# Kernel tuning notes

Hardware: AMD Instinct MI355X
Metric: run time of the kernel (lower is better)

The kernel has to match this reference:

```python
import jax, jax.numpy as jnp
import numpy as np

QP = 127.0          # 2**(8-1)-1, signed symmetric int8
MIN_RANGE = 1e-6


def _ste_round(x):
    # round_pass: forward round, straight-through gradient
    return x + jax.lax.stop_gradient(jnp.round(x) - x)


def _quant_per_tensor(x):
    # symmetric per-tensor: scale = max|x| / Qp (grad flows through max as in source)
    scale = jnp.maximum(jnp.max(jnp.abs(x)), MIN_RANGE) / QP
    return _ste_round(x / scale), scale


def _qlinear(x2d, w, b):
    # faithful to _quantize_global (prefix_token_num=None path):
    #   out = (x_q @ w_q.T + bias) * (s_w * s_x)
    xq, sx = _quant_per_tensor(x2d)
    wq, sw = _quant_per_tensor(w)
    out = jnp.matmul(xq, wq.T) + b[None, :]
    return out * (sw * sx)


def setup_inputs() -> dict:
    key = jax.random.key(0)
    k = jax.random.split(key, 5)
    B, N, D, H = 8, 1024, 1024, 4096
    return {
        "x": jax.random.normal(k[0], (B, N, D), dtype=jnp.float32),
        "w1": jax.random.normal(k[1], (H, D), dtype=jnp.float32) * 0.02,
        "b1": jax.random.normal(k[2], (H,), dtype=jnp.float32) * 0.02,
        "w2": jax.random.normal(k[3], (D, H), dtype=jnp.float32) * 0.02,
        "b2": jax.random.normal(k[4], (D,), dtype=jnp.float32) * 0.02,
    }


def reference(x, w1, b1, w2, b2):
    B, N, D = x.shape
    h = _qlinear(x.reshape(-1, D), w1, b1)          # [B*N, H]
    h = jax.nn.gelu(h, approximate=False)            # exact GELU (nn.GELU default)
    o = _qlinear(h, w2, b2)                          # [B*N, D]
    return o.reshape(B, N, -1)
```

## Files before the change

### kernel.cpp

```cpp
#include <hip/hip_runtime.h>
#include <cstdint>
#include <cmath>

#define QP    127.0f
#define MINR  1e-6f

#define MTOK 8192
#define DDIM 1024
#define HDIM 4096

typedef __attribute__((ext_vector_type(4))) int int32x4;

__device__ __forceinline__ void gload16(const void* g, void* l) {
    __builtin_amdgcn_global_load_lds(
        (const __attribute__((address_space(1))) void*)g,
        (__attribute__((address_space(3))) void*)l, 16, 0, 0);
}

__global__ void zero_scales_kernel(float* g) {
    if (threadIdx.x < 4) g[threadIdx.x] = 0.0f;
}

__global__ void absmax_kernel(const float* __restrict__ in, int n4, float* __restrict__ gout) {
    const float4* in4 = (const float4*)in;
    int tid = blockIdx.x * blockDim.x + threadIdx.x;
    int stride = gridDim.x * blockDim.x;
    float m = 0.0f;
    for (int i = tid; i < n4; i += stride) {
        float4 v = in4[i];
        m = fmaxf(m, fmaxf(fmaxf(fabsf(v.x), fabsf(v.y)), fmaxf(fabsf(v.z), fabsf(v.w))));
    }
    #pragma unroll
    for (int off = 32; off; off >>= 1) m = fmaxf(m, __shfl_down(m, off));
    __shared__ float sm[4];
    int lane = threadIdx.x & 63, w = threadIdx.x >> 6;
    if (lane == 0) sm[w] = m;
    __syncthreads();
    if (threadIdx.x == 0) {
        float bm = fmaxf(fmaxf(sm[0], sm[1]), fmaxf(sm[2], sm[3]));
        atomicMax((int*)gout, __float_as_int(bm));
    }
}

__global__ void quant_kernel(const float* __restrict__ in, int8_t* __restrict__ out,
                             int n4, const float* __restrict__ gm) {
    const float s = fmaxf(*gm, MINR) / QP;
    const float4* in4 = (const float4*)in;
    int* out4 = (int*)out;
    int tid = blockIdx.x * blockDim.x + threadIdx.x;
    int stride = gridDim.x * blockDim.x;
    for (int i = tid; i < n4; i += stride) {
        float4 v = in4[i];
        int q0 = ((int)rintf(v.x / s)) & 255;
        int q1 = ((int)rintf(v.y / s)) & 255;
        int q2 = ((int)rintf(v.z / s)) & 255;
        int q3 = ((int)rintf(v.w / s)) & 255;
        out4[i] = q0 | (q1 << 8) | (q2 << 16) | (q3 << 24);
    }
}

template<int KD, int ND, bool GELU_EPI>
__global__ __launch_bounds__(256, 2)
void gemm_i8_kernel(const int8_t* __restrict__ A, const int8_t* __restrict__ B,
                    const float* __restrict__ bias,
                    const float* __restrict__ gmA, const float* __restrict__ gmB,
                    float* __restrict__ out, float* __restrict__ omax) {
    __shared__ int8_t lA[128 * 128];
    __shared__ int8_t lB[128 * 128];
    const int t = threadIdx.x;
    const int lane = t & 63;
    const int w = t >> 6;
    const int wm = (w >> 1) * 64;
    const int wn = (w & 1) * 64;
    const int lr = lane & 15;
    const int lg = lane >> 4;
    const int br = blockIdx.y, bc = blockIdx.x;

    const int8_t* Ab = A + (size_t)br * 128 * KD;
    const int8_t* Bb = B + (size_t)bc * 128 * KD;

    int32x4 acc[4][4] = {};

    for (int kt = 0; kt < KD / 128; ++kt) {
        #pragma unroll
        for (int i = 0; i < 4; ++i) {
            int c = t + i * 256;
            int r = c >> 3;
            int sl = c & 7;
            int sc = ((sl ^ (r & 7)) << 4);
            gload16(Ab + (size_t)r * KD + kt * 128 + sc, &lA[c * 16]);
            gload16(Bb + (size_t)r * KD + kt * 128 + sc, &lB[c * 16]);
        }
        __syncthreads();

        #pragma unroll
        for (int kk = 0; kk < 2; ++kk) {
            int32x4 af[4], bf[4];
            #pragma unroll
            for (int m = 0; m < 4; ++m) {
                int r = wm + m * 16 + lr;
                int g = kk * 4 + lg;
                af[m] = *(const int32x4*)&lA[r * 128 + ((g ^ (r & 7)) << 4)];
            }
            #pragma unroll
            for (int n = 0; n < 4; ++n) {
                int r = wn + n * 16 + lr;
                int g = kk * 4 + lg;
                bf[n] = *(const int32x4*)&lB[r * 128 + ((g ^ (r & 7)) << 4)];
            }
            #pragma unroll
            for (int m = 0; m < 4; ++m)
                #pragma unroll
                for (int n = 0; n < 4; ++n)
                    acc[m][n] = __builtin_amdgcn_mfma_i32_16x16x64_i8(af[m], bf[n], acc[m][n], 0, 0, 0);
        }
        __syncthreads();
    }

    const float sA = fmaxf(*gmA, MINR) / QP;
    const float sB = fmaxf(*gmB, MINR) / QP;
    const float s = sB * sA;
    float lmax = 0.0f;
    #pragma unroll
    for (int m = 0; m < 4; ++m) {
        #pragma unroll
        for (int n = 0; n < 4; ++n) {
            #pragma unroll
            for (int r = 0; r < 4; ++r) {
                int row = br * 128 + wm + m * 16 + lg * 4 + r;
                int col = bc * 128 + wn + n * 16 + lr;
                float f = (float)acc[m][n][r] + bias[col];
                f *= s;
                if (GELU_EPI) {
                    float gg = f * (erff(f / 1.41421356237309504880f) + 1.0f) * 0.5f;
                    out[(size_t)row * ND + col] = gg;
                    lmax = fmaxf(lmax, fabsf(gg));
                } else {
                    out[(size_t)row * ND + col] = f;
                }
            }
        }
    }
    if (GELU_EPI) {
        #pragma unroll
        for (int off = 32; off; off >>= 1) lmax = fmaxf(lmax, __shfl_down(lmax, off));
        __shared__ float red[4];
        if (lane == 0) red[w] = lmax;
        __syncthreads();
        if (t == 0) {
            float bm = fmaxf(fmaxf(red[0], red[1]), fmaxf(red[2], red[3]));
            atomicMax((int*)omax, __float_as_int(bm));
        }
    }
}

extern "C" void kernel_launch(void* const* d_in, const int* in_sizes, int n_in,
                              void* d_out, int out_size, void* d_ws, size_t ws_size,
                              hipStream_t stream) {
    const float* x  = (const float*)d_in[0];
    const float* w1 = (const float*)d_in[1];
    const float* b1 = (const float*)d_in[2];
    const float* w2 = (const float*)d_in[3];
    const float* b2 = (const float*)d_in[4];
    float* out = (float*)d_out;

    uint8_t* ws = (uint8_t*)d_ws;
    float*  gmax = (float*)ws;
    int8_t* xq   = (int8_t*)(ws + 256);
    int8_t* w1q  = xq  + (size_t)MTOK * DDIM;
    int8_t* w2q  = w1q + (size_t)HDIM * DDIM;
    int8_t* hq   = w2q + (size_t)DDIM * HDIM;
    float*  h    = (float*)(hq + (size_t)MTOK * HDIM);

    zero_scales_kernel<<<1, 64, 0, stream>>>(gmax);

    absmax_kernel<<<1024, 256, 0, stream>>>(x,  MTOK * DDIM / 4, gmax + 0);
    absmax_kernel<<<512,  256, 0, stream>>>(w1, HDIM * DDIM / 4, gmax + 1);
    absmax_kernel<<<512,  256, 0, stream>>>(w2, DDIM * HDIM / 4, gmax + 3);

    quant_kernel<<<2048, 256, 0, stream>>>(x,  xq,  MTOK * DDIM / 4, gmax + 0);
    quant_kernel<<<1024, 256, 0, stream>>>(w1, w1q, HDIM * DDIM / 4, gmax + 1);
    quant_kernel<<<1024, 256, 0, stream>>>(w2, w2q, DDIM * HDIM / 4, gmax + 3);

    gemm_i8_kernel<DDIM, HDIM, true>
        <<<dim3(HDIM / 128, MTOK / 128), 256, 0, stream>>>(xq, w1q, b1, gmax + 0, gmax + 1, h, gmax + 2);

    quant_kernel<<<4096, 256, 0, stream>>>(h, hq, MTOK * HDIM / 4, gmax + 2);

    gemm_i8_kernel<HDIM, DDIM, false>
        <<<dim3(DDIM / 128, MTOK / 128), 256, 0, stream>>>(hq, w2q, b2, gmax + 2, gmax + 3, out, nullptr);
}
```

Measured before the change: 211.0 us.

## Merge absmax/quant launches, remap GEMM blocks for XCD locality, raise occupancy

```diff
diff --git a/kernel.cpp b/kernel.cpp
--- a/kernel.cpp
+++ b/kernel.cpp
@@ -21,34 +21,44 @@
     if (threadIdx.x < 4) g[threadIdx.x] = 0.0f;
 }
 
-__global__ void absmax_kernel(const float* __restrict__ in, int n4, float* __restrict__ gout) {
-    const float4* in4 = (const float4*)in;
-    int tid = blockIdx.x * blockDim.x + threadIdx.x;
-    int stride = gridDim.x * blockDim.x;
-    float m = 0.0f;
-    for (int i = tid; i < n4; i += stride) {
-        float4 v = in4[i];
-        m = fmaxf(m, fmaxf(fmaxf(fabsf(v.x), fabsf(v.y)), fmaxf(fabsf(v.z), fabsf(v.w))));
-    }
+__device__ __forceinline__ float wave_block_max(float m) {
     #pragma unroll
     for (int off = 32; off; off >>= 1) m = fmaxf(m, __shfl_down(m, off));
     __shared__ float sm[4];
     int lane = threadIdx.x & 63, w = threadIdx.x >> 6;
     if (lane == 0) sm[w] = m;
     __syncthreads();
-    if (threadIdx.x == 0) {
-        float bm = fmaxf(fmaxf(sm[0], sm[1]), fmaxf(sm[2], sm[3]));
-        atomicMax((int*)gout, __float_as_int(bm));
-    }
-}
-
-__global__ void quant_kernel(const float* __restrict__ in, int8_t* __restrict__ out,
-                             int n4, const float* __restrict__ gm) {
+    float bm = 0.0f;
+    if (threadIdx.x == 0) bm = fmaxf(fmaxf(sm[0], sm[1]), fmaxf(sm[2], sm[3]));
+    return bm;
+}
+
+__device__ __forceinline__ void absmax_range(const float4* in4, int n4, int bid, int nb,
+                                             float* gout) {
+    int tid = bid * blockDim.x + threadIdx.x;
+    int stride = nb * blockDim.x;
+    float m = 0.0f;
+    for (int i = tid; i < n4; i += stride) {
+        float4 v = in4[i];
+        m = fmaxf(m, fmaxf(fmaxf(fabsf(v.x), fabsf(v.y)), fmaxf(fabsf(v.z), fabsf(v.w))));
+    }
+    float bm = wave_block_max(m);
+    if (threadIdx.x == 0) atomicMax((int*)gout, __float_as_int(bm));
+}
+
+__global__ void absmax3_kernel(const float* __restrict__ x, const float* __restrict__ w1,
+                               const float* __restrict__ w2, float* __restrict__ gmax) {
+    int b = blockIdx.x;
+    if (b < 1024)      absmax_range((const float4*)x,  MTOK * DDIM / 4, b,        1024, gmax + 0);
+    else if (b < 1536) absmax_range((const float4*)w1, HDIM * DDIM / 4, b - 1024,  512, gmax + 1);
+    else               absmax_range((const float4*)w2, DDIM * HDIM / 4, b - 1536,  512, gmax + 3);
+}
+
+__device__ __forceinline__ void quant_range(const float4* in4, int* out4, int n4,
+                                            int bid, int nb, const float* gm) {
     const float s = fmaxf(*gm, MINR) / QP;
-    const float4* in4 = (const float4*)in;
-    int* out4 = (int*)out;
-    int tid = blockIdx.x * blockDim.x + threadIdx.x;
-    int stride = gridDim.x * blockDim.x;
+    int tid = bid * blockDim.x + threadIdx.x;
+    int stride = nb * blockDim.x;
     for (int i = tid; i < n4; i += stride) {
         float4 v = in4[i];
         int q0 = ((int)rintf(v.x / s)) & 255;
@@ -59,8 +69,23 @@
     }
 }
 
+__global__ void quant3_kernel(const float* __restrict__ x, const float* __restrict__ w1,
+                              const float* __restrict__ w2, int8_t* __restrict__ xq,
+                              int8_t* __restrict__ w1q, int8_t* __restrict__ w2q,
+                              const float* __restrict__ gmax) {
+    int b = blockIdx.x;
+    if (b < 2048)      quant_range((const float4*)x,  (int*)xq,  MTOK * DDIM / 4, b,        2048, gmax + 0);
+    else if (b < 3072) quant_range((const float4*)w1, (int*)w1q, HDIM * DDIM / 4, b - 2048, 1024, gmax + 1);
+    else               quant_range((const float4*)w2, (int*)w2q, DDIM * HDIM / 4, b - 3072, 1024, gmax + 3);
+}
+
+__global__ void quant_kernel(const float* __restrict__ in, int8_t* __restrict__ out,
+                             int n4, const float* __restrict__ gm) {
+    quant_range((const float4*)in, (int*)out, n4, blockIdx.x, gridDim.x, gm);
+}
+
 template<int KD, int ND, bool GELU_EPI>
-__global__ __launch_bounds__(256, 2)
+__global__ __launch_bounds__(256, 3)
 void gemm_i8_kernel(const int8_t* __restrict__ A, const int8_t* __restrict__ B,
                     const float* __restrict__ bias,
                     const float* __restrict__ gmA, const float* __restrict__ gmB,
@@ -74,7 +99,11 @@
     const int wn = (w & 1) * 64;
     const int lr = lane & 15;
     const int lg = lane >> 4;
-    const int br = blockIdx.y, bc = blockIdx.x;
+
+    const int chunk = gridDim.x >> 3;
+    const int logical = (blockIdx.x & 7) * chunk + (blockIdx.x >> 3);
+    const int br = logical & 63;
+    const int bc = logical >> 6;
 
     const int8_t* Ab = A + (size_t)br * 128 * KD;
     const int8_t* Bb = B + (size_t)bc * 128 * KD;
@@ -174,19 +203,14 @@
 
     zero_scales_kernel<<<1, 64, 0, stream>>>(gmax);
 
-    absmax_kernel<<<1024, 256, 0, stream>>>(x,  MTOK * DDIM / 4, gmax + 0);
-    absmax_kernel<<<512,  256, 0, stream>>>(w1, HDIM * DDIM / 4, gmax + 1);
-    absmax_kernel<<<512,  256, 0, stream>>>(w2, DDIM * HDIM / 4, gmax + 3);
-
-    quant_kernel<<<2048, 256, 0, stream>>>(x,  xq,  MTOK * DDIM / 4, gmax + 0);
-    quant_kernel<<<1024, 256, 0, stream>>>(w1, w1q, HDIM * DDIM / 4, gmax + 1);
-    quant_kernel<<<1024, 256, 0, stream>>>(w2, w2q, DDIM * HDIM / 4, gmax + 3);
+    absmax3_kernel<<<2048, 256, 0, stream>>>(x, w1, w2, gmax);
+    quant3_kernel<<<4096, 256, 0, stream>>>(x, w1, w2, xq, w1q, w2q, gmax);
 
     gemm_i8_kernel<DDIM, HDIM, true>
-        <<<dim3(HDIM / 128, MTOK / 128), 256, 0, stream>>>(xq, w1q, b1, gmax + 0, gmax + 1, h, gmax + 2);
+        <<<2048, 256, 0, stream>>>(xq, w1q, b1, gmax + 0, gmax + 1, h, gmax + 2);
 
     quant_kernel<<<4096, 256, 0, stream>>>(h, hq, MTOK * HDIM / 4, gmax + 2);
 
     gemm_i8_kernel<HDIM, DDIM, false>
-        <<<dim3(DDIM / 128, MTOK / 128), 256, 0, stream>>>(hq, w2q, b2, gmax + 2, gmax + 3, out, nullptr);
-}
+        <<<512, 256, 0, stream>>>(hq, w2q, b2, gmax + 2, gmax + 3, out, nullptr);
+}
```

New measurement: 208.3 us. About the same (-1.3%).
